# Performance work log

Hardware: AMD Instinct MI355X
Metric: run time of the kernel (lower is better)

## Reference

```python
import jax, jax.numpy as jnp
import numpy as np

N_ATOMS = 50_000
N_PAIRS = 1_000_000
F_A = 75    # n_atom_input_feat
F_P = 14    # n_pair_input_feat
H = 50      # all hidden / output widths


def _glorot(key, shape):
    fan_in, fan_out = shape
    lim = np.sqrt(6.0 / (fan_in + fan_out)).astype(np.float32)
    return jax.random.uniform(key, shape, jnp.float32, -lim, lim)


def setup_inputs() -> dict:
    key = jax.random.key(0)
    ks = jax.random.split(key, 12)
    atom_features = jax.random.normal(ks[0], (N_ATOMS, F_A), jnp.float32)
    pair_features = jax.random.normal(ks[1], (N_PAIRS, F_P), jnp.float32)
    # per-pair anchor-atom segment id (sorted, as pairs are grouped by atom)
    pair_seg = jnp.sort(jax.random.randint(ks[2], (N_PAIRS,), 0, N_ATOMS, jnp.int32))
    atom_to_pair = jax.random.randint(ks[3], (N_PAIRS, 2), 0, N_ATOMS, jnp.int32)
    return {
        "atom_features": atom_features,
        "pair_features": pair_features,
        "pair_seg": pair_seg,
        "atom_to_pair": atom_to_pair,
        "W_AA": _glorot(ks[4], (F_A, H)), "b_AA": jnp.zeros((H,), jnp.float32),
        "W_PA": _glorot(ks[5], (F_P, H)), "b_PA": jnp.zeros((H,), jnp.float32),
        "W_A": _glorot(ks[6], (2 * H, H)), "b_A": jnp.zeros((H,), jnp.float32),
        "W_AP": _glorot(ks[7], (2 * F_A, H)), "b_AP": jnp.zeros((H,), jnp.float32),
        "W_PP": _glorot(ks[8], (F_P, H)), "b_PP": jnp.zeros((H,), jnp.float32),
        "W_P": _glorot(ks[9], (2 * H, H)), "b_P": jnp.zeros((H,), jnp.float32),
    }


def reference(atom_features, pair_features, pair_seg, atom_to_pair,
              W_AA, b_AA, W_PA, b_PA, W_A, b_A, W_AP, b_AP, W_PP, b_PP, W_P, b_P):
    act = jax.nn.relu
    n_atoms = atom_features.shape[0]
    n_pairs = pair_features.shape[0]

    # atom -> atom
    AA = act(atom_features @ W_AA + b_AA)                              # [Na, H]
    # pair -> atom: per-pair hidden, segment-summed to the anchor atom
    PA = act(pair_features @ W_PA + b_PA)                              # [Np, H]
    PA_sum = jax.ops.segment_sum(PA, pair_seg, num_segments=n_atoms)   # [Na, H]
    A = act(jnp.concatenate([AA, PA_sum], axis=1) @ W_A + b_A)         # [Na, H]

    # atom -> pair: gather both endpoints, (i,j) and (j,i) orderings
    ap = atom_features[atom_to_pair]                                   # [Np, 2, Fa]
    AP_ij = act(ap.reshape(n_pairs, 2 * ap.shape[-1]) @ W_AP + b_AP)
    AP_ji = act(ap[:, ::-1, :].reshape(n_pairs, 2 * ap.shape[-1]) @ W_AP + b_AP)
    # pair -> pair
    PP = act(pair_features @ W_PP + b_PP)
    P = act(jnp.concatenate([AP_ij + AP_ji, PP], axis=1) @ W_P + b_P)  # [Np, H]
    return A, P
```

## Files before the change

### kernel.cpp

```cpp
#include <hip/hip_runtime.h>
#include <hip/hip_bf16.h>

#define NA 50000
#define NP 1000000
#define FA 75
#define FP 14
#define H  50

typedef __attribute__((ext_vector_type(8))) short short8;
typedef __attribute__((ext_vector_type(4))) float f32x4;

__device__ __forceinline__ ushort f2bf(float f) {
    union { float f; unsigned u; } v; v.f = f;
    unsigned r = v.u + 0x7FFF + ((v.u >> 16) & 1);
    return (ushort)(r >> 16);
}
__device__ __forceinline__ unsigned cvtpk(float lo, float hi) {
    unsigned r;
    asm("v_cvt_pk_bf16_f32 %0, %1, %2" : "=v"(r) : "v"(lo), "v"(hi));
    return r;
}
__device__ __forceinline__ ushort f2bf1(float f) { return (ushort)cvtpk(f, f); }
__device__ __forceinline__ unsigned pk_fp8(float u, float v) {
    unsigned r;
    asm("v_cvt_pk_fp8_f32 %0, %1, %2" : "=v"(r) : "v"(u), "v"(v));
    return r;
}
__device__ __forceinline__ float2 unpk_fp8(unsigned w) {
    float2 r;
    asm("v_cvt_pk_f32_fp8 %0, %1" : "=v"(r) : "v"(w));
    return r;
}
__device__ __forceinline__ short8 mk8(unsigned a, unsigned b, unsigned c, unsigned d) {
    union { unsigned u[4]; short8 s; } x; x.u[0]=a; x.u[1]=b; x.u[2]=c; x.u[3]=d; return x.s;
}

__global__ __launch_bounds__(256) void k_prep_frags(
    const float* __restrict__ W_P, const float* __restrict__ W_A,
    const float* __restrict__ W_PP, const float* __restrict__ W_PA,
    const float* __restrict__ W_AA, const float* __restrict__ W_AP,
    ushort* __restrict__ WPf, ushort* __restrict__ WAf, ushort* __restrict__ W2f,
    ushort* __restrict__ WPREf)
{
    const int t0 = blockIdx.x * 256 + threadIdx.x;
    const int STR = 16 * 256;
    for (int idx = t0; idx < 4*4*64*8; idx += STR) {
        int j = idx & 7, l = (idx >> 3) & 63, tn = (idx >> 9) & 3, tk = idx >> 11;
        int k = tk*32 + (l>>4)*8 + j;
        int c = tn*16 + (l&15);
        ushort vp = 0, va = 0;
        if (k < 100 && c < 50) { vp = f2bf(W_P[k*50+c]); va = f2bf(W_A[k*50+c]); }
        WPf[idx] = vp; WAf[idx] = va;
    }
    for (int idx = t0; idx < 8*64*8; idx += STR) {
        int j = idx & 7, l = (idx >> 3) & 63, tn = idx >> 9;
        int k = (l>>4)*8 + j;
        int c = (tn&3)*16 + (l&15);
        ushort v = 0;
        if (k < 14 && c < 50) v = f2bf(tn < 4 ? W_PP[k*50+c] : W_PA[k*50+c]);
        W2f[idx] = v;
    }
    for (int idx = t0; idx < 3*12*64*8; idx += STR) {
        int j = idx & 7, l = (idx >> 3) & 63;
        int g = idx >> 9;
        int tn = g % 12, tk = g / 12;
        int k = tk*32 + (l>>4)*8 + j;
        int sn = tn*16 + (l&15);
        int which = sn >> 6, col = sn & 63;
        ushort v = 0;
        if (k < FA && col < H) {
            float w = (which == 0) ? W_AA[k*H+col]
                    : (which == 1) ? W_AP[k*H+col]
                                   : W_AP[(FA+k)*H+col];
            v = f2bf(w);
        }
        WPREf[idx] = v;
    }
}

__global__ __launch_bounds__(256) void k_atom_pre(
    const float* __restrict__ af, const ushort* __restrict__ WPREf,
    const float* __restrict__ b_AA,
    ushort* __restrict__ AAb, ushort* __restrict__ UV8)
{
    __shared__ __align__(16) ushort sAF[64][104];
    const int t = threadIdx.x, lane = t & 63, w = t >> 6;
    const int a0 = blockIdx.x * 64, row0 = w * 16;

    for (int idx = t; idx < 64*96; idx += 256) {
        int r = idx / 96, c = idx % 96;
        int ag = a0 + r;
        float v = (c < FA && ag < NA) ? af[(size_t)ag*FA + c] : 0.f;
        sAF[r][c] = f2bf(v);
    }
    __syncthreads();

    short8 afr[3];
    #pragma unroll
    for (int tk = 0; tk < 3; ++tk)
        afr[tk] = *(const short8*)&sAF[row0 + (lane&15)][tk*32 + (lane>>4)*8];

    const short8* B = (const short8*)WPREf;
    f32x4 acc[12];
    #pragma unroll
    for (int tn = 0; tn < 12; ++tn) acc[tn] = (f32x4){0.f, 0.f, 0.f, 0.f};
    #pragma unroll
    for (int tk = 0; tk < 3; ++tk) {
        #pragma unroll
        for (int tn = 0; tn < 12; ++tn) {
            short8 b = B[(tk*12 + tn)*64 + lane];
            acc[tn] = __builtin_amdgcn_mfma_f32_16x16x32_bf16(afr[tk], b, acc[tn], 0, 0, 0);
        }
    }

    #pragma unroll
    for (int tn = 0; tn < 4; ++tn) {
        int col = tn*16 + (lane&15);
        if (col < H) {
            float ba = b_AA[col];
            #pragma unroll
            for (int reg = 0; reg < 4; ++reg) {
                int atom = a0 + row0 + (lane>>4)*4 + reg;
                if (atom < NA) {
                    AAb[(size_t)atom*H + col] = f2bf(fmaxf(acc[tn][reg] + ba, 0.f));
                    UV8[(size_t)atom*64 + col] =
                        (ushort)pk_fp8(acc[4 + tn][reg], acc[8 + tn][reg]);
                }
            }
        }
    }
}

__global__ __launch_bounds__(256, 4) void k_pairs(
    const float* __restrict__ pf, const int* __restrict__ seg, const int* __restrict__ a2p,
    const ushort* __restrict__ UV8,
    const float* __restrict__ b_PP, const float* __restrict__ b_PA,
    const float* __restrict__ b_AP, const float* __restrict__ b_P,
    const ushort* __restrict__ WPf, const ushort* __restrict__ W2f,
    float* __restrict__ PAsum, float* __restrict__ Pout)
{
    __shared__ __align__(16) ushort sX[64][136];

    const int t = threadIdx.x;
    const int w = t >> 6, lane = t & 63;
    const int q = lane >> 4, m = lane & 15;
    const int p0 = blockIdx.x * 64;
    const int row0 = w * 16;
    const int p0w_u = __builtin_amdgcn_readfirstlane(p0 + row0);

    const int* a2ps = a2p + 2 * p0w_u;
    const int* segs = seg + p0w_u;
    int pi[16], pj[16], sg[16];
    #pragma unroll
    for (int it = 0; it < 16; ++it) {
        pi[it] = a2ps[2*it];
        pj[it] = a2ps[2*it + 1];
        sg[it] = segs[it];
    }

    const float2* pf2 = (const float2*)(pf + (size_t)(p0w_u + m) * FP);
    float2 g0 = {0.f,0.f}, g1 = {0.f,0.f}, g2 = {0.f,0.f}, g3 = {0.f,0.f};
    if (q == 0)      { g0 = pf2[0]; g1 = pf2[1]; g2 = pf2[2]; g3 = pf2[3]; }
    else if (q == 1) { g0 = pf2[4]; g1 = pf2[5]; g2 = pf2[6]; }
    short8 afrag = mk8(cvtpk(g0.x, g0.y), cvtpk(g1.x, g1.y),
                       cvtpk(g2.x, g2.y), cvtpk(g3.x, g3.y));

    unsigned uvi[16], uvj[16];
    const unsigned lo2 = (unsigned)(lane << 1);
    #pragma unroll
    for (int it = 0; it < 16; ++it) {
        unsigned offi = ((unsigned)pi[it] << 7) | lo2;
        unsigned offj = ((unsigned)pj[it] << 7) | lo2;
        asm volatile("global_load_ushort %0, %1, %2"
                     : "=v"(uvi[it]) : "v"(offi), "s"(UV8));
        asm volatile("global_load_ushort %0, %1, %2"
                     : "=v"(uvj[it]) : "v"(offj), "s"(UV8));
    }

    if (lane < 16) {
        unsigned long long* rowp = (unsigned long long*)&sX[row0 + lane][100];
        #pragma unroll
        for (int d = 0; d < 7; ++d) rowp[d] = 0ull;
    }
    float bap = (lane < H) ? b_AP[lane] : 0.f;

    asm volatile("s_waitcnt vmcnt(0)" ::: "memory");
    __builtin_amdgcn_sched_barrier(0);

    #pragma unroll
    for (int it = 0; it < 16; ++it) {
        if (lane < H) {
            float2 fi = unpk_fp8(uvi[it]);
            float2 fj = unpk_fp8(uvj[it]);
            float aps = fmaxf(fi.x + fj.y + bap, 0.f) + fmaxf(fj.x + fi.y + bap, 0.f);
            sX[row0 + it][lane] = f2bf1(aps);
        }
    }

    float pa[4][4];
    {
        const short8* B = (const short8*)W2f;
        #pragma unroll
        for (int tn = 0; tn < 8; ++tn) {
            f32x4 c = {0.f, 0.f, 0.f, 0.f};
            short8 b = B[tn*64 + lane];
            c = __builtin_amdgcn_mfma_f32_16x16x32_bf16(afrag, b, c, 0, 0, 0);
            int col = (tn&3)*16 + m;
            if (tn < 4) {
                if (col < H) {
                    float bias = b_PP[col];
                    #pragma unroll
                    for (int reg = 0; reg < 4; ++reg)
                        sX[row0 + q*4 + reg][H + col] = f2bf1(fmaxf(c[reg] + bias, 0.f));
                }
            } else {
                float bias = (col < H) ? b_PA[col] : 0.f;
                #pragma unroll
                for (int reg = 0; reg < 4; ++reg)
                    pa[tn-4][reg] = fmaxf(c[reg] + bias, 0.f);
            }
        }
    }

    #pragma unroll
    for (int tn4 = 0; tn4 < 4; ++tn4) {
        float v[16];
        #pragma unroll
        for (int g = 0; g < 4; ++g) {
            int src = m + (g << 4);
            #pragma unroll
            for (int r4 = 0; r4 < 4; ++r4)
                v[g*4 + r4] = __shfl(pa[tn4][r4], src, 64);
        }
        int col = tn4*16 + m;
        if (q == 0 && col < H) {
            float acc = v[0]; int cur = sg[0];
            #pragma unroll
            for (int r = 1; r < 16; ++r) {
                if (sg[r] != cur) {
                    atomicAdd(&PAsum[(size_t)cur*H + col], acc);
                    acc = 0.f; cur = sg[r];
                }
                acc += v[r];
            }
            atomicAdd(&PAsum[(size_t)cur*H + col], acc);
        }
    }

    asm volatile("s_waitcnt lgkmcnt(0)" ::: "memory");
    __builtin_amdgcn_sched_barrier(0);

    {
        short8 afr[4];
        #pragma unroll
        for (int tk = 0; tk < 4; ++tk)
            afr[tk] = *(const short8*)&sX[row0 + m][tk*32 + q*8];
        const short8* B = (const short8*)WPf;
        f32x4 acc[4];
        #pragma unroll
        for (int tn = 0; tn < 4; ++tn) acc[tn] = (f32x4){0.f, 0.f, 0.f, 0.f};
        #pragma unroll
        for (int tk = 0; tk < 4; ++tk) {
            #pragma unroll
            for (int tn = 0; tn < 4; ++tn) {
                short8 b = B[(tk*4 + tn)*64 + lane];
                acc[tn] = __builtin_amdgcn_mfma_f32_16x16x32_bf16(afr[tk], b, acc[tn], 0, 0, 0);
            }
        }
        #pragma unroll
        for (int tn = 0; tn < 4; ++tn) {
            int col = tn*16 + m;
            if (col < H) {
                float bp = b_P[col];
                #pragma unroll
                for (int reg = 0; reg < 4; ++reg) {
                    int row = row0 + q*4 + reg;
                    Pout[(size_t)(p0 + row)*H + col] = fmaxf(acc[tn][reg] + bp, 0.f);
                }
            }
        }
    }
}

__global__ __launch_bounds__(256) void k_A(
    const ushort* __restrict__ AAb, const float* __restrict__ PAsum,
    const ushort* __restrict__ WAf, const float* __restrict__ b_A,
    float* __restrict__ Aout)
{
    __shared__ __align__(16) ushort sX[64][136];
    const int t = threadIdx.x, lane = t & 63, w = t >> 6;
    const int a0 = blockIdx.x * 64;
    const int row0 = w * 16;

    for (int idx = t; idx < 64*50; idx += 256) {
        int r = idx / 50, c = idx % 50;
        int rg = a0 + r;
        ushort aa = 0; float ps = 0.f;
        if (rg < NA) { aa = AAb[(size_t)rg*H + c]; ps = PAsum[(size_t)rg*H + c]; }
        sX[r][c] = aa;
        sX[r][H + c] = f2bf1(ps);
    }
    for (int idx = t; idx < 64*28; idx += 256) {
        int r = idx / 28, c = 100 + idx % 28;
        sX[r][c] = 0;
    }
    __syncthreads();

    short8 afr[4];
    #pragma unroll
    for (int tk = 0; tk < 4; ++tk)
        afr[tk] = *(const short8*)&sX[row0 + (lane&15)][tk*32 + (lane>>4)*8];
    const short8* B = (const short8*)WAf;
    f32x4 acc[4];
    #pragma unroll
    for (int tn = 0; tn < 4; ++tn) acc[tn] = (f32x4){0.f, 0.f, 0.f, 0.f};
    #pragma unroll
    for (int tk = 0; tk < 4; ++tk) {
        #pragma unroll
        for (int tn = 0; tn < 4; ++tn) {
            short8 b = B[(tk*4 + tn)*64 + lane];
            acc[tn] = __builtin_amdgcn_mfma_f32_16x16x32_bf16(afr[tk], b, acc[tn], 0, 0, 0);
        }
    }
    #pragma unroll
    for (int tn = 0; tn < 4; ++tn) {
        int col = tn*16 + (lane&15);
        if (col < H) {
            float ba = b_A[col];
            #pragma unroll
            for (int reg = 0; reg < 4; ++reg) {
                int row = row0 + (lane>>4)*4 + reg;
                int rg = a0 + row;
                if (rg < NA) Aout[(size_t)rg*H + col] = fmaxf(acc[tn][reg] + ba, 0.f);
            }
        }
    }
}

extern "C" void kernel_launch(void* const* d_in, const int* in_sizes, int n_in,
                              void* d_out, int out_size, void* d_ws, size_t ws_size,
                              hipStream_t stream)
{
    const float* af   = (const float*)d_in[0];
    const float* pf   = (const float*)d_in[1];
    const int*   seg  = (const int*)d_in[2];
    const int*   a2p  = (const int*)d_in[3];
    const float* W_AA = (const float*)d_in[4];
    const float* b_AA = (const float*)d_in[5];
    const float* W_PA = (const float*)d_in[6];
    const float* b_PA = (const float*)d_in[7];
    const float* W_A  = (const float*)d_in[8];
    const float* b_A  = (const float*)d_in[9];
    const float* W_AP = (const float*)d_in[10];
    const float* b_AP = (const float*)d_in[11];
    const float* W_PP = (const float*)d_in[12];
    const float* b_PP = (const float*)d_in[13];
    const float* W_P  = (const float*)d_in[14];
    const float* b_P  = (const float*)d_in[15];

    float* Aout = (float*)d_out;
    float* Pout = (float*)d_out + (size_t)NA * H;

    ushort*   AAb   = (ushort*)d_ws;
    float*    PAsum = (float*)(AAb + (size_t)NA * H);
    ushort*   UV8   = (ushort*)(PAsum + (size_t)NA * H);
    ushort*   WPf   = UV8 + (size_t)NA * 64;
    ushort*   WAf   = WPf + 4*4*64*8;
    ushort*   W2f   = WAf + 4*4*64*8;
    ushort*   WPREf = W2f + 8*64*8;

    hipMemsetAsync(PAsum, 0, (size_t)NA * H * sizeof(float), stream);
    k_prep_frags<<<16, 256, 0, stream>>>(W_P, W_A, W_PP, W_PA, W_AA, W_AP,
                                         WPf, WAf, W2f, WPREf);
    k_atom_pre<<<(NA + 63) / 64, 256, 0, stream>>>(af, WPREf, b_AA, AAb, UV8);
    k_pairs<<<NP / 64, 256, 0, stream>>>(pf, seg, a2p, UV8, b_PP, b_PA, b_AP, b_P,
                                         WPf, W2f, PAsum, Pout);
    k_A<<<(NA + 63) / 64, 256, 0, stream>>>(AAb, PAsum, WAf, b_A, Aout);
}
```

Before: 211.2 us.

## Restructure pair kernel: two strips per wave, register-resident weights, folded biases

The pair kernel now runs 128-thread blocks, with each wave handling two 16-pair strips. The MFMA weight fragments are loaded once into registers and reused for both strips. UV8 gathers use dword loads split between the i and j lanes, then redistribute with ds_bpermute, and the second strip's loads overlap the first strip's compute. Biases are folded into the weight fragments through a constant-one input column (k=100 / k=14), which removes the bias loads and adds in the epilogues. Segment-sum atomics are done per lane-quad without cross-lane shuffles, which may issue more atomics; register pressure rises sharply from holding 24 weight fragments.

```diff
diff --git a/kernel.cpp b/kernel.cpp
--- a/kernel.cpp
+++ b/kernel.cpp
@@ -34,11 +34,16 @@
 __device__ __forceinline__ short8 mk8(unsigned a, unsigned b, unsigned c, unsigned d) {
     union { unsigned u[4]; short8 s; } x; x.u[0]=a; x.u[1]=b; x.u[2]=c; x.u[3]=d; return x.s;
 }
+__device__ __forceinline__ float asf(unsigned u) {
+    union { unsigned u; float f; } v; v.u = u; return v.f;
+}
 
 __global__ __launch_bounds__(256) void k_prep_frags(
     const float* __restrict__ W_P, const float* __restrict__ W_A,
     const float* __restrict__ W_PP, const float* __restrict__ W_PA,
     const float* __restrict__ W_AA, const float* __restrict__ W_AP,
+    const float* __restrict__ b_PP, const float* __restrict__ b_PA,
+    const float* __restrict__ b_P, const float* __restrict__ b_A,
     ushort* __restrict__ WPf, ushort* __restrict__ WAf, ushort* __restrict__ W2f,
     ushort* __restrict__ WPREf)
 {
@@ -49,7 +54,10 @@
         int k = tk*32 + (l>>4)*8 + j;
         int c = tn*16 + (l&15);
         ushort vp = 0, va = 0;
-        if (k < 100 && c < 50) { vp = f2bf(W_P[k*50+c]); va = f2bf(W_A[k*50+c]); }
+        if (c < 50) {
+            if (k < 100)       { vp = f2bf(W_P[k*50+c]); va = f2bf(W_A[k*50+c]); }
+            else if (k == 100) { vp = f2bf(b_P[c]);      va = f2bf(b_A[c]); }
+        }
         WPf[idx] = vp; WAf[idx] = va;
     }
     for (int idx = t0; idx < 8*64*8; idx += STR) {
@@ -57,7 +65,10 @@
         int k = (l>>4)*8 + j;
         int c = (tn&3)*16 + (l&15);
         ushort v = 0;
-        if (k < 14 && c < 50) v = f2bf(tn < 4 ? W_PP[k*50+c] : W_PA[k*50+c]);
+        if (c < 50) {
+            if (k < 14)       v = f2bf(tn < 4 ? W_PP[k*50+c] : W_PA[k*50+c]);
+            else if (k == 14) v = f2bf(tn < 4 ? b_PP[c] : b_PA[c]);
+        }
         W2f[idx] = v;
     }
     for (int idx = t0; idx < 3*12*64*8; idx += STR) {
@@ -69,10 +80,10 @@
         int which = sn >> 6, col = sn & 63;
         ushort v = 0;
         if (k < FA && col < H) {
-            float w = (which == 0) ? W_AA[k*H+col]
-                    : (which == 1) ? W_AP[k*H+col]
-                                   : W_AP[(FA+k)*H+col];
-            v = f2bf(w);
+            float wv = (which == 0) ? W_AA[k*H+col]
+                     : (which == 1) ? W_AP[k*H+col]
+                                    : W_AP[(FA+k)*H+col];
+            v = f2bf(wv);
         }
         WPREf[idx] = v;
     }
@@ -131,161 +142,183 @@
     }
 }
 
-__global__ __launch_bounds__(256, 4) void k_pairs(
+__global__ __launch_bounds__(128) void k_pairs(
     const float* __restrict__ pf, const int* __restrict__ seg, const int* __restrict__ a2p,
-    const ushort* __restrict__ UV8,
-    const float* __restrict__ b_PP, const float* __restrict__ b_PA,
-    const float* __restrict__ b_AP, const float* __restrict__ b_P,
+    const ushort* __restrict__ UV8, const float* __restrict__ b_AP,
     const ushort* __restrict__ WPf, const ushort* __restrict__ W2f,
     float* __restrict__ PAsum, float* __restrict__ Pout)
 {
-    __shared__ __align__(16) ushort sX[64][136];
-
-    const int t = threadIdx.x;
-    const int w = t >> 6, lane = t & 63;
+    __shared__ __align__(16) ushort sX[32][136];
+    const int t = threadIdx.x, w = t >> 6, lane = t & 63;
     const int q = lane >> 4, m = lane & 15;
-    const int p0 = blockIdx.x * 64;
     const int row0 = w * 16;
-    const int p0w_u = __builtin_amdgcn_readfirstlane(p0 + row0);
-
-    const int* a2ps = a2p + 2 * p0w_u;
-    const int* segs = seg + p0w_u;
-    int pi[16], pj[16], sg[16];
-    #pragma unroll
-    for (int it = 0; it < 16; ++it) {
-        pi[it] = a2ps[2*it];
-        pj[it] = a2ps[2*it + 1];
-        sg[it] = segs[it];
-    }
-
-    const float2* pf2 = (const float2*)(pf + (size_t)(p0w_u + m) * FP);
-    float2 g0 = {0.f,0.f}, g1 = {0.f,0.f}, g2 = {0.f,0.f}, g3 = {0.f,0.f};
-    if (q == 0)      { g0 = pf2[0]; g1 = pf2[1]; g2 = pf2[2]; g3 = pf2[3]; }
-    else if (q == 1) { g0 = pf2[4]; g1 = pf2[5]; g2 = pf2[6]; }
-    short8 afrag = mk8(cvtpk(g0.x, g0.y), cvtpk(g1.x, g1.y),
-                       cvtpk(g2.x, g2.y), cvtpk(g3.x, g3.y));
-
-    unsigned uvi[16], uvj[16];
-    const unsigned lo2 = (unsigned)(lane << 1);
-    #pragma unroll
-    for (int it = 0; it < 16; ++it) {
-        unsigned offi = ((unsigned)pi[it] << 7) | lo2;
-        unsigned offj = ((unsigned)pj[it] << 7) | lo2;
-        asm volatile("global_load_ushort %0, %1, %2"
-                     : "=v"(uvi[it]) : "v"(offi), "s"(UV8));
-        asm volatile("global_load_ushort %0, %1, %2"
-                     : "=v"(uvj[it]) : "v"(offj), "s"(UV8));
+    const int pb_u = __builtin_amdgcn_readfirstlane(blockIdx.x * 64 + w * 32);
+
+    const int* a2ps = a2p + 2 * pb_u;
+    int pi[32], pj[32];
+    #pragma unroll
+    for (int i = 0; i < 32; ++i) { pi[i] = a2ps[2*i]; pj[i] = a2ps[2*i+1]; }
+
+    unsigned bap_u;
+    { unsigned voff = (unsigned)((lane < 50 ? lane : 49) << 2);
+      asm volatile("global_load_dword %0, %1, %2" : "=v"(bap_u) : "v"(voff), "s"(b_AP)); }
+    short8 wf2[8];
+    #pragma unroll
+    for (int i = 0; i < 8; ++i) {
+        unsigned voff = (unsigned)((i*64 + lane) * 16);
+        asm volatile("global_load_dwordx4 %0, %1, %2" : "=v"(wf2[i]) : "v"(voff), "s"(W2f));
+    }
+    short8 wfP[16];
+    #pragma unroll
+    for (int i = 0; i < 16; ++i) {
+        unsigned voff = (unsigned)((i*64 + lane) * 16);
+        asm volatile("global_load_dwordx4 %0, %1, %2" : "=v"(wfP[i]) : "v"(voff), "s"(WPf));
+    }
+    const bool isJ = (lane >= 32);
+    const unsigned dsel = (unsigned)((lane & 31) << 2);
+    unsigned uv0[16], uv1[16];
+    #pragma unroll
+    for (int i = 0; i < 16; ++i) {
+        int row = isJ ? pj[i] : pi[i];
+        unsigned voff = ((unsigned)row << 7) | dsel;
+        asm volatile("global_load_dword %0, %1, %2" : "=v"(uv0[i]) : "v"(voff), "s"(UV8));
+    }
+    f32x4 pfA0, pfB0;
+    { unsigned rb = (unsigned)(pb_u + m) * 56u;
+      unsigned va = rb + (q == 1 ? 32u : 0u);
+      unsigned vb = rb + (q == 1 ? 40u : 16u);
+      asm volatile("global_load_dwordx4 %0, %1, %2" : "=v"(pfA0) : "v"(va), "s"(pf));
+      asm volatile("global_load_dwordx4 %0, %1, %2" : "=v"(pfB0) : "v"(vb), "s"(pf));
+    }
+    #pragma unroll
+    for (int i = 0; i < 16; ++i) {
+        int row = isJ ? pj[16+i] : pi[16+i];
+        unsigned voff = ((unsigned)row << 7) | dsel;
+        asm volatile("global_load_dword %0, %1, %2" : "=v"(uv1[i]) : "v"(voff), "s"(UV8));
+    }
+    f32x4 pfA1, pfB1;
+    { unsigned rb = (unsigned)(pb_u + 16 + m) * 56u;
+      unsigned va = rb + (q == 1 ? 32u : 0u);
+      unsigned vb = rb + (q == 1 ? 40u : 16u);
+      asm volatile("global_load_dwordx4 %0, %1, %2" : "=v"(pfA1) : "v"(va), "s"(pf));
+      asm volatile("global_load_dwordx4 %0, %1, %2" : "=v"(pfB1) : "v"(vb), "s"(pf));
     }
 
     if (lane < 16) {
         unsigned long long* rowp = (unsigned long long*)&sX[row0 + lane][100];
-        #pragma unroll
-        for (int d = 0; d < 7; ++d) rowp[d] = 0ull;
-    }
-    float bap = (lane < H) ? b_AP[lane] : 0.f;
-
-    asm volatile("s_waitcnt vmcnt(0)" ::: "memory");
-    __builtin_amdgcn_sched_barrier(0);
-
-    #pragma unroll
-    for (int it = 0; it < 16; ++it) {
-        if (lane < H) {
-            float2 fi = unpk_fp8(uvi[it]);
-            float2 fj = unpk_fp8(uvj[it]);
-            float aps = fmaxf(fi.x + fj.y + bap, 0.f) + fmaxf(fj.x + fi.y + bap, 0.f);
-            sX[row0 + it][lane] = f2bf1(aps);
-        }
-    }
-
-    float pa[4][4];
-    {
-        const short8* B = (const short8*)W2f;
+        rowp[0] = 0x0000000000003F80ull;
+        #pragma unroll
+        for (int d = 1; d < 7; ++d) rowp[d] = 0ull;
+    }
+
+    const int addrA = (lane >> 1) << 2;
+    const int addrB = addrA + 128;
+
+    auto STRIP = [&](const unsigned (&uvp)[16], const f32x4& pfA, const f32x4& pfB,
+                     int sbase_u) {
+        unsigned w0 = cvtpk(pfA.x, pfA.y);
+        unsigned w1 = cvtpk(pfA.z, pfA.w);
+        unsigned w2 = (q == 1) ? cvtpk(pfB.z, pfB.w) : cvtpk(pfB.x, pfB.y);
+        unsigned w3 = (q == 0) ? cvtpk(pfB.z, pfB.w) : ((q == 1) ? 0x00003F80u : 0u);
+        if (q >= 2) { w0 = 0; w1 = 0; w2 = 0; }
+        short8 afrag = mk8(w0, w1, w2, w3);
+        float bapf = asf(bap_u);
+
+        #pragma unroll
+        for (int it = 0; it < 16; ++it) {
+            unsigned va = (unsigned)__builtin_amdgcn_ds_bpermute(addrA, (int)uvp[it]);
+            unsigned vb = (unsigned)__builtin_amdgcn_ds_bpermute(addrB, (int)uvp[it]);
+            unsigned sh = (unsigned)((lane & 1) << 4);
+            float2 fi = unpk_fp8(va >> sh);
+            float2 fj = unpk_fp8(vb >> sh);
+            float aps = fmaxf(fi.x + fj.y + bapf, 0.f) + fmaxf(fj.x + fi.y + bapf, 0.f);
+            if (lane < H) sX[row0 + it][lane] = f2bf1(aps);
+        }
+
+        float pa[4][4];
         #pragma unroll
         for (int tn = 0; tn < 8; ++tn) {
             f32x4 c = {0.f, 0.f, 0.f, 0.f};
-            short8 b = B[tn*64 + lane];
-            c = __builtin_amdgcn_mfma_f32_16x16x32_bf16(afrag, b, c, 0, 0, 0);
+            c = __builtin_amdgcn_mfma_f32_16x16x32_bf16(afrag, wf2[tn], c, 0, 0, 0);
             int col = (tn&3)*16 + m;
             if (tn < 4) {
                 if (col < H) {
-                    float bias = b_PP[col];
                     #pragma unroll
                     for (int reg = 0; reg < 4; ++reg)
-                        sX[row0 + q*4 + reg][H + col] = f2bf1(fmaxf(c[reg] + bias, 0.f));
+                        sX[row0 + q*4 + reg][H + col] = f2bf1(fmaxf(c[reg], 0.f));
                 }
             } else {
-                float bias = (col < H) ? b_PA[col] : 0.f;
                 #pragma unroll
                 for (int reg = 0; reg < 4; ++reg)
-                    pa[tn-4][reg] = fmaxf(c[reg] + bias, 0.f);
+                    pa[tn-4][reg] = fmaxf(c[reg], 0.f);
             }
         }
-    }
-
-    #pragma unroll
-    for (int tn4 = 0; tn4 < 4; ++tn4) {
-        float v[16];
-        #pragma unroll
-        for (int g = 0; g < 4; ++g) {
-            int src = m + (g << 4);
-            #pragma unroll
-            for (int r4 = 0; r4 < 4; ++r4)
-                v[g*4 + r4] = __shfl(pa[tn4][r4], src, 64);
-        }
-        int col = tn4*16 + m;
-        if (q == 0 && col < H) {
-            float acc = v[0]; int cur = sg[0];
-            #pragma unroll
-            for (int r = 1; r < 16; ++r) {
-                if (sg[r] != cur) {
-                    atomicAdd(&PAsum[(size_t)cur*H + col], acc);
-                    acc = 0.f; cur = sg[r];
-                }
-                acc += v[r];
-            }
-            atomicAdd(&PAsum[(size_t)cur*H + col], acc);
-        }
-    }
-
-    asm volatile("s_waitcnt lgkmcnt(0)" ::: "memory");
-    __builtin_amdgcn_sched_barrier(0);
-
-    {
+
+        const int* sgp = seg + sbase_u;
+        int sg[16];
+        #pragma unroll
+        for (int i = 0; i < 16; ++i) sg[i] = sgp[i];
+        int s0 = q==0 ? sg[0] : q==1 ? sg[4] : q==2 ? sg[8]  : sg[12];
+        int s1 = q==0 ? sg[1] : q==1 ? sg[5] : q==2 ? sg[9]  : sg[13];
+        int s2 = q==0 ? sg[2] : q==1 ? sg[6] : q==2 ? sg[10] : sg[14];
+        int s3 = q==0 ? sg[3] : q==1 ? sg[7] : q==2 ? sg[11] : sg[15];
+        #pragma unroll
+        for (int tn4 = 0; tn4 < 4; ++tn4) {
+            int col = tn4*16 + m;
+            bool act = col < H;
+            float acc = pa[tn4][0]; int cur = s0;
+            if (s1 != cur) { if (act) atomicAdd(&PAsum[(size_t)cur*H + col], acc); acc = 0.f; cur = s1; }
+            acc += pa[tn4][1];
+            if (s2 != cur) { if (act) atomicAdd(&PAsum[(size_t)cur*H + col], acc); acc = 0.f; cur = s2; }
+            acc += pa[tn4][2];
+            if (s3 != cur) { if (act) atomicAdd(&PAsum[(size_t)cur*H + col], acc); acc = 0.f; cur = s3; }
+            acc += pa[tn4][3];
+            if (act) atomicAdd(&PAsum[(size_t)cur*H + col], acc);
+        }
+
+        asm volatile("s_waitcnt lgkmcnt(0)" ::: "memory");
+        __builtin_amdgcn_sched_barrier(0);
+
         short8 afr[4];
         #pragma unroll
         for (int tk = 0; tk < 4; ++tk)
             afr[tk] = *(const short8*)&sX[row0 + m][tk*32 + q*8];
-        const short8* B = (const short8*)WPf;
-        f32x4 acc[4];
-        #pragma unroll
-        for (int tn = 0; tn < 4; ++tn) acc[tn] = (f32x4){0.f, 0.f, 0.f, 0.f};
+        f32x4 acc4[4];
+        #pragma unroll
+        for (int tn = 0; tn < 4; ++tn) acc4[tn] = (f32x4){0.f, 0.f, 0.f, 0.f};
         #pragma unroll
         for (int tk = 0; tk < 4; ++tk) {
             #pragma unroll
-            for (int tn = 0; tn < 4; ++tn) {
-                short8 b = B[(tk*4 + tn)*64 + lane];
-                acc[tn] = __builtin_amdgcn_mfma_f32_16x16x32_bf16(afr[tk], b, acc[tn], 0, 0, 0);
-            }
+            for (int tn = 0; tn < 4; ++tn)
+                acc4[tn] = __builtin_amdgcn_mfma_f32_16x16x32_bf16(afr[tk], wfP[tk*4+tn], acc4[tn], 0, 0, 0);
         }
         #pragma unroll
         for (int tn = 0; tn < 4; ++tn) {
             int col = tn*16 + m;
             if (col < H) {
-                float bp = b_P[col];
                 #pragma unroll
                 for (int reg = 0; reg < 4; ++reg) {
-                    int row = row0 + q*4 + reg;
-                    Pout[(size_t)(p0 + row)*H + col] = fmaxf(acc[tn][reg] + bp, 0.f);
+                    int prow = sbase_u + q*4 + reg;
+                    Pout[(size_t)prow*H + col] = fmaxf(acc4[tn][reg], 0.f);
                 }
             }
         }
-    }
+    };
+
+    asm volatile("s_waitcnt vmcnt(18)" ::: "memory");
+    __builtin_amdgcn_sched_barrier(0);
+    STRIP(uv0, pfA0, pfB0, pb_u);
+
+    asm volatile("s_waitcnt vmcnt(0)" ::: "memory");
+    __builtin_amdgcn_sched_barrier(0);
+    asm volatile("s_waitcnt lgkmcnt(0)" ::: "memory");
+    __builtin_amdgcn_sched_barrier(0);
+    STRIP(uv1, pfA1, pfB1, pb_u + 16);
 }
 
 __global__ __launch_bounds__(256) void k_A(
     const ushort* __restrict__ AAb, const float* __restrict__ PAsum,
-    const ushort* __restrict__ WAf, const float* __restrict__ b_A,
-    float* __restrict__ Aout)
+    const ushort* __restrict__ WAf, float* __restrict__ Aout)
 {
     __shared__ __align__(16) ushort sX[64][136];
     const int t = threadIdx.x, lane = t & 63, w = t >> 6;
@@ -302,7 +335,7 @@
     }
     for (int idx = t; idx < 64*28; idx += 256) {
         int r = idx / 28, c = 100 + idx % 28;
-        sX[r][c] = 0;
+        sX[r][c] = (c == 100) ? (ushort)0x3F80 : (ushort)0;
     }
     __syncthreads();
 
@@ -326,12 +359,11 @@
     for (int tn = 0; tn < 4; ++tn) {
         int col = tn*16 + (lane&15);
         if (col < H) {
-            float ba = b_A[col];
             #pragma unroll
             for (int reg = 0; reg < 4; ++reg) {
                 int row = row0 + (lane>>4)*4 + reg;
                 int rg = a0 + row;
-                if (rg < NA) Aout[(size_t)rg*H + col] = fmaxf(acc[tn][reg] + ba, 0.f);
+                if (rg < NA) Aout[(size_t)rg*H + col] = fmaxf(acc[tn][reg], 0.f);
             }
         }
     }
@@ -371,9 +403,10 @@
 
     hipMemsetAsync(PAsum, 0, (size_t)NA * H * sizeof(float), stream);
     k_prep_frags<<<16, 256, 0, stream>>>(W_P, W_A, W_PP, W_PA, W_AA, W_AP,
+                                         b_PP, b_PA, b_P, b_A,
                                          WPf, WAf, W2f, WPREf);
     k_atom_pre<<<(NA + 63) / 64, 256, 0, stream>>>(af, WPREf, b_AA, AAb, UV8);
-    k_pairs<<<NP / 64, 256, 0, stream>>>(pf, seg, a2p, UV8, b_PP, b_PA, b_AP, b_P,
+    k_pairs<<<NP / 64, 128, 0, stream>>>(pf, seg, a2p, UV8, b_AP,
                                          WPf, W2f, PAsum, Pout);
-    k_A<<<(NA + 63) / 64, 256, 0, stream>>>(AAb, PAsum, WAf, b_A, Aout);
-}
+    k_A<<<(NA + 63) / 64, 256, 0, stream>>>(AAb, PAsum, WAf, Aout);
+}
```

Result: slower. 270.4 us (+28.0%).

## Use nontemporal loads/stores for streamed data and split gather wait into two halves

Applied to the files above, without the earlier changes.

Marks streamed inputs (atom features, pair features, AA and PA sums) and outputs (P, A) as nontemporal so they are less likely to pollute cache, which leaves more room for the reused UV8 gather table. The 32 gathered ushort loads are now waited on in two halves using vmcnt(16), so the first 8 rows are unpacked and written while the second half is still in flight. The pair-feature loads and bias load are hoisted ahead of the gathers, and the bf16 packing is deferred. This can raise register pressure, and the nontemporal hints may change L2 behavior in unexpected ways.

```diff
diff --git a/kernel.cpp b/kernel.cpp
--- a/kernel.cpp
+++ b/kernel.cpp
@@ -9,6 +9,7 @@
 
 typedef __attribute__((ext_vector_type(8))) short short8;
 typedef __attribute__((ext_vector_type(4))) float f32x4;
+typedef __attribute__((ext_vector_type(2))) float f32x2;
 
 __device__ __forceinline__ ushort f2bf(float f) {
     union { float f; unsigned u; } v; v.f = f;
@@ -90,7 +91,7 @@
     for (int idx = t; idx < 64*96; idx += 256) {
         int r = idx / 96, c = idx % 96;
         int ag = a0 + r;
-        float v = (c < FA && ag < NA) ? af[(size_t)ag*FA + c] : 0.f;
+        float v = (c < FA && ag < NA) ? __builtin_nontemporal_load(&af[(size_t)ag*FA + c]) : 0.f;
         sAF[r][c] = f2bf(v);
     }
     __syncthreads();
@@ -158,17 +159,25 @@
         sg[it] = segs[it];
     }
 
-    const float2* pf2 = (const float2*)(pf + (size_t)(p0w_u + m) * FP);
-    float2 g0 = {0.f,0.f}, g1 = {0.f,0.f}, g2 = {0.f,0.f}, g3 = {0.f,0.f};
-    if (q == 0)      { g0 = pf2[0]; g1 = pf2[1]; g2 = pf2[2]; g3 = pf2[3]; }
-    else if (q == 1) { g0 = pf2[4]; g1 = pf2[5]; g2 = pf2[6]; }
-    short8 afrag = mk8(cvtpk(g0.x, g0.y), cvtpk(g1.x, g1.y),
-                       cvtpk(g2.x, g2.y), cvtpk(g3.x, g3.y));
+    const f32x2* pf2 = (const f32x2*)(pf + (size_t)(p0w_u + m) * FP);
+    f32x2 g0 = {0.f,0.f}, g1 = {0.f,0.f}, g2 = {0.f,0.f}, g3 = {0.f,0.f};
+    if (q == 0) {
+        g0 = __builtin_nontemporal_load(&pf2[0]);
+        g1 = __builtin_nontemporal_load(&pf2[1]);
+        g2 = __builtin_nontemporal_load(&pf2[2]);
+        g3 = __builtin_nontemporal_load(&pf2[3]);
+    } else if (q == 1) {
+        g0 = __builtin_nontemporal_load(&pf2[4]);
+        g1 = __builtin_nontemporal_load(&pf2[5]);
+        g2 = __builtin_nontemporal_load(&pf2[6]);
+    }
+    float bap = (lane < H) ? b_AP[lane] : 0.f;
+    __builtin_amdgcn_sched_barrier(0);
 
     unsigned uvi[16], uvj[16];
     const unsigned lo2 = (unsigned)(lane << 1);
     #pragma unroll
-    for (int it = 0; it < 16; ++it) {
+    for (int it = 0; it < 8; ++it) {
         unsigned offi = ((unsigned)pi[it] << 7) | lo2;
         unsigned offj = ((unsigned)pj[it] << 7) | lo2;
         asm volatile("global_load_ushort %0, %1, %2"
@@ -176,19 +185,26 @@
         asm volatile("global_load_ushort %0, %1, %2"
                      : "=v"(uvj[it]) : "v"(offj), "s"(UV8));
     }
+    #pragma unroll
+    for (int it = 8; it < 16; ++it) {
+        unsigned offi = ((unsigned)pi[it] << 7) | lo2;
+        unsigned offj = ((unsigned)pj[it] << 7) | lo2;
+        asm volatile("global_load_ushort %0, %1, %2"
+                     : "=v"(uvi[it]) : "v"(offi), "s"(UV8));
+        asm volatile("global_load_ushort %0, %1, %2"
+                     : "=v"(uvj[it]) : "v"(offj), "s"(UV8));
+    }
 
     if (lane < 16) {
         unsigned long long* rowp = (unsigned long long*)&sX[row0 + lane][100];
         #pragma unroll
         for (int d = 0; d < 7; ++d) rowp[d] = 0ull;
     }
-    float bap = (lane < H) ? b_AP[lane] : 0.f;
-
-    asm volatile("s_waitcnt vmcnt(0)" ::: "memory");
+
+    asm volatile("s_waitcnt vmcnt(16)" ::: "memory");
     __builtin_amdgcn_sched_barrier(0);
-
-    #pragma unroll
-    for (int it = 0; it < 16; ++it) {
+    #pragma unroll
+    for (int it = 0; it < 8; ++it) {
         if (lane < H) {
             float2 fi = unpk_fp8(uvi[it]);
             float2 fj = unpk_fp8(uvj[it]);
@@ -196,7 +212,20 @@
             sX[row0 + it][lane] = f2bf1(aps);
         }
     }
-
+    asm volatile("s_waitcnt vmcnt(0)" ::: "memory");
+    __builtin_amdgcn_sched_barrier(0);
+    #pragma unroll
+    for (int it = 8; it < 16; ++it) {
+        if (lane < H) {
+            float2 fi = unpk_fp8(uvi[it]);
+            float2 fj = unpk_fp8(uvj[it]);
+            float aps = fmaxf(fi.x + fj.y + bap, 0.f) + fmaxf(fj.x + fi.y + bap, 0.f);
+            sX[row0 + it][lane] = f2bf1(aps);
+        }
+    }
+
+    short8 afrag = mk8(cvtpk(g0.x, g0.y), cvtpk(g1.x, g1.y),
+                       cvtpk(g2.x, g2.y), cvtpk(g3.x, g3.y));
     float pa[4][4];
     {
         const short8* B = (const short8*)W2f;
@@ -275,7 +304,8 @@
                 #pragma unroll
                 for (int reg = 0; reg < 4; ++reg) {
                     int row = row0 + q*4 + reg;
-                    Pout[(size_t)(p0 + row)*H + col] = fmaxf(acc[tn][reg] + bp, 0.f);
+                    __builtin_nontemporal_store(fmaxf(acc[tn][reg] + bp, 0.f),
+                                                &Pout[(size_t)(p0 + row)*H + col]);
                 }
             }
         }
@@ -296,7 +326,10 @@
         int r = idx / 50, c = idx % 50;
         int rg = a0 + r;
         ushort aa = 0; float ps = 0.f;
-        if (rg < NA) { aa = AAb[(size_t)rg*H + c]; ps = PAsum[(size_t)rg*H + c]; }
+        if (rg < NA) {
+            aa = __builtin_nontemporal_load(&AAb[(size_t)rg*H + c]);
+            ps = __builtin_nontemporal_load(&PAsum[(size_t)rg*H + c]);
+        }
         sX[r][c] = aa;
         sX[r][H + c] = f2bf1(ps);
     }
@@ -331,7 +364,9 @@
             for (int reg = 0; reg < 4; ++reg) {
                 int row = row0 + (lane>>4)*4 + reg;
                 int rg = a0 + row;
-                if (rg < NA) Aout[(size_t)rg*H + col] = fmaxf(acc[tn][reg] + ba, 0.f);
+                if (rg < NA)
+                    __builtin_nontemporal_store(fmaxf(acc[tn][reg] + ba, 0.f),
+                                                &Aout[(size_t)rg*H + col]);
             }
         }
     }
```

After: 254.7 us. +20.6%, slower.
